# Performance work log

Hardware: AMD Instinct MI355X
Metric: run time of the kernel (lower is better)

Reference implementation:

```python
import jax, jax.numpy as jnp
import numpy as np

KS = 3          # kernel_size
NUM_FA = 16     # number of functional atoms per pixel
TOTAL_BASES = 6 # num_bases * (ks // 2)
BN_EPS = 1e-5


def _conv3x3(x, w, b):
    # NCHW conv, padding=1, stride=1
    y = jax.lax.conv_general_dilated(
        x, w, window_strides=(1, 1), padding=[(1, 1), (1, 1)],
        dimension_numbers=("NCHW", "OIHW", "NCHW"))
    return y + b[None, :, None, None]


def _bn(x, gamma, beta, mean, var):
    scale = gamma / jnp.sqrt(var + BN_EPS)
    return (x - mean[None, :, None, None]) * scale[None, :, None, None] + beta[None, :, None, None]


def setup_inputs() -> dict:
    key = jax.random.key(0)
    ks = jax.random.split(key, 16)
    N, C, H, W = 16, 64, 64, 64
    INTER, BC_DIM, O = 64, TOTAL_BASES * NUM_FA, 128
    f32 = jnp.float32
    return {
        "x": jax.random.normal(ks[0], (N, C, H, W), f32),
        "conv1_w": jax.random.normal(ks[1], (INTER, C, 3, 3), f32) * 0.05,
        "conv1_b": jax.random.normal(ks[2], (INTER,), f32) * 0.05,
        "bn1_gamma": jax.random.uniform(ks[3], (INTER,), f32, 0.5, 1.5),
        "bn1_beta": jax.random.normal(ks[4], (INTER,), f32) * 0.05,
        "bn1_mean": jax.random.normal(ks[5], (INTER,), f32) * 0.05,
        "bn1_var": jax.random.uniform(ks[6], (INTER,), f32, 0.5, 1.5),
        "conv2_w": jax.random.normal(ks[7], (BC_DIM, INTER, 3, 3), f32) * 0.05,
        "conv2_b": jax.random.normal(ks[8], (BC_DIM,), f32) * 0.05,
        "bn2_gamma": jax.random.uniform(ks[9], (BC_DIM,), f32, 0.5, 1.5),
        "bn2_beta": jax.random.normal(ks[10], (BC_DIM,), f32) * 0.05,
        "bn2_mean": jax.random.normal(ks[11], (BC_DIM,), f32) * 0.05,
        "bn2_var": jax.random.uniform(ks[12], (BC_DIM,), f32, 0.5, 1.5),
        "bases": jax.random.normal(ks[13], (TOTAL_BASES, KS * KS), f32),
        "coef": jax.random.normal(ks[14], (O, C * NUM_FA), f32) * 0.02,
    }


def reference(x, conv1_w, conv1_b, bn1_gamma, bn1_beta, bn1_mean, bn1_var,
              conv2_w, conv2_b, bn2_gamma, bn2_beta, bn2_mean, bn2_var,
              bases, coef):
    N, C, H, W = x.shape
    # bases_net: conv3x3 -> BN -> tanh -> conv3x3 -> BN -> tanh
    h = jnp.tanh(_bn(_conv3x3(x, conv1_w, conv1_b), bn1_gamma, bn1_beta, bn1_mean, bn1_var))
    bc = jnp.tanh(_bn(_conv3x3(h, conv2_w, conv2_b), bn2_gamma, bn2_beta, bn2_mean, bn2_var))
    # torch: .transpose(1,-1).view(N,H,W,num_fa,total_bases)  (swaps H/W; H==W)
    bases_coef = jnp.transpose(bc, (0, 3, 2, 1)).reshape(N, H, W, NUM_FA, TOTAL_BASES)
    # atoms: (bases_coef[...,None] * bases).sum(-2).transpose(-1,-2) -> (N,H,W,ks2,num_fa)
    atoms = jnp.einsum("nhwft,tk->nhwkf", bases_coef, bases)
    # unfold(x, ks, padding=1) -> patches (N,H,W,C,ks2), channel-major like torch unfold
    xp = jnp.pad(x, ((0, 0), (0, 0), (1, 1), (1, 1)))
    patches = jnp.stack([xp[:, :, i:i + H, j:j + W] for i in range(KS) for j in range(KS)], axis=2)  # (N,C,9,H,W)
    patches = jnp.transpose(patches, (0, 3, 4, 1, 2))  # (N,H,W,C,9)
    # (x.unsqueeze(-1) * atoms.unsqueeze(-3)).sum(-2) -> (N,H,W,C,num_fa) -> flatten C-major
    bases_out = jnp.einsum("nhwck,nhwkf->nhwcf", patches, atoms).reshape(N, H, W, C * NUM_FA)
    # torch: .transpose(1,-1) -> (N, C*num_fa, W, H), then 1x1 conv with coef
    out = jnp.einsum("nhwd,od->nowh", bases_out, coef)  # (N, O, W, H)
    return out
```

## Files before the change

### kernel.cpp

```cpp
#include <hip/hip_runtime.h>
#include <math.h>
#include <string.h>

#define NBATCH 16

typedef __attribute__((ext_vector_type(8))) short short8;
typedef __attribute__((ext_vector_type(4))) float floatx4;
typedef __fp16 half2v __attribute__((ext_vector_type(2)));
#define MFMA16(a, b, c) __builtin_amdgcn_mfma_f32_16x16x32_bf16(a, b, c, 0, 0, 0)

__device__ __forceinline__ unsigned int cvtpk(float a, float b) {
  unsigned int r;
  asm("v_cvt_pk_bf16_f32 %0, %1, %2" : "=v"(r) : "v"(a), "v"(b));
  return r;
}
__device__ __forceinline__ unsigned short f2bf(float f) {
  return (unsigned short)(cvtpk(f, 0.f) & 0xffffu);
}
__device__ __forceinline__ unsigned int packbf2(float a, float b) {
  return cvtpk(a, b);
}
__device__ __forceinline__ float bflo(unsigned int u) {
  return __uint_as_float(u << 16);
}
__device__ __forceinline__ float bfhi(unsigned int u) {
  return __uint_as_float(u & 0xffff0000u);
}
__device__ __forceinline__ float fast_tanh(float x) {
  float e = __expf(2.f * x);
  return 1.f - 2.f / (e + 1.f);
}

__global__ void prep_weights(const float* __restrict__ w1,
                             const float* __restrict__ w2,
                             const float* __restrict__ coef,
                             unsigned short* __restrict__ w1swz,
                             unsigned short* __restrict__ w2swz,
                             unsigned short* __restrict__ coefswz) {
  int i = blockIdx.x * 256 + threadIdx.x;
  if (i < 131072) {
    int j = i & 7, f = i >> 3;
    int lane = f & 63;
    int u = (f >> 6) & 3;
    int wj = (f >> 8) & 1;
    int kc = (f >> 9) & 1;
    int rd = f >> 10;
    int lm = lane & 15, lq = lane >> 4;
    int oc = wj * 64 + u * 16 + lm;
    int k = rd * 64 + kc * 32 + lq * 8 + j;
    coefswz[i] = f2bf(coef[oc * 1024 + k]);
  }
  if (i < 36864) {
    int j = i & 7, f = i >> 3;
    int lane = f & 63;
    int u = (f >> 6) & 1;
    int wn = (f >> 7) & 1;
    int kc = (f >> 8) & 1;
    int off = f >> 9;
    int lm = lane & 15, lq = lane >> 4;
    int oc = wn * 32 + u * 16 + lm;
    int ic = kc * 32 + lq * 8 + j;
    w1swz[i] = f2bf(w1[(oc * 64 + ic) * 9 + off]);
  }
  if (i < 55296) {
    int j = i & 7, f = i >> 3;
    int lane = f & 63;
    int rem = f >> 6;
    int u = rem % 3;
    int rem2 = rem / 3;
    int wn = rem2 & 1;
    int kc = (rem2 >> 1) & 1;
    int off = rem2 >> 2;
    int lm = lane & 15, lq = lane >> 4;
    int oc = wn * 48 + u * 16 + lm;
    int ic = kc * 32 + lq * 8 + j;
    w2swz[i] = f2bf(w2[(oc * 64 + ic) * 9 + off]);
  }
}

__global__ __launch_bounds__(256) void xb_prep(const float* __restrict__ x,
                                               unsigned short* __restrict__ xb) {
  __shared__ float tile[64][65];
  const int t = threadIdx.x;
  const int y = blockIdx.x, n = blockIdx.y;
  const float* xn = x + (size_t)n * 64 * 4096 + y * 64;
#pragma unroll
  for (int it = 0; it < 16; ++it) {
    int idx = it * 256 + t;
    int c = idx >> 6, xx = idx & 63;
    tile[c][xx] = xn[c * 4096 + xx];
  }
  __syncthreads();
  const int xx = t >> 2, cq = t & 3;
  unsigned short* dst = xb + ((size_t)n * 4096 + y * 64 + xx) * 64;
#pragma unroll
  for (int jj = 0; jj < 2; ++jj) {
    int ch0 = cq * 16 + jj * 8;
    unsigned int p[4];
#pragma unroll
    for (int e = 0; e < 4; ++e)
      p[e] = packbf2(tile[ch0 + e * 2][xx], tile[ch0 + e * 2 + 1][xx]);
    *(uint4*)&dst[ch0] = make_uint4(p[0], p[1], p[2], p[3]);
  }
}

__global__ __launch_bounds__(256) void fused_conv(
    const unsigned short* __restrict__ xb, const unsigned short* __restrict__ w1swz,
    const unsigned short* __restrict__ w2swz, const float* __restrict__ b1,
    const float* __restrict__ g1, const float* __restrict__ be1,
    const float* __restrict__ m1, const float* __restrict__ v1,
    const float* __restrict__ b2, const float* __restrict__ g2,
    const float* __restrict__ be2, const float* __restrict__ m2,
    const float* __restrict__ v2, unsigned short* __restrict__ bcg) {
  __shared__ unsigned short xls[144 * 72];
  __shared__ unsigned short hls[128 * 72];

  const int t = threadIdx.x;
  const int tile = blockIdx.x, n = blockIdx.y;
  const int x0 = (tile & 7) * 8, y0 = (tile >> 3) * 8;

  const unsigned short* xbn = xb + (size_t)n * 4096 * 64;
#pragma unroll
  for (int it = 0; it < 5; ++it) {
    int idx = it * 256 + t;
    if (idx < 1152) {
      int pos = idx >> 3, u4 = idx & 7;
      int xr = pos / 12, xc = pos - xr * 12;
      int gy = y0 - 2 + xr, gx = x0 - 2 + xc;
      uint4 v = {0u, 0u, 0u, 0u};
      if ((unsigned)gy < 64u && (unsigned)gx < 64u)
        v = *(const uint4*)&xbn[((size_t)gy * 64 + gx) * 64 + u4 * 8];
      *(uint4*)&xls[pos * 72 + u4 * 8] = v;
    }
  }
  __syncthreads();

  const int lane = t & 63, w = t >> 6;
  const int wm = w & 1, wn = w >> 1;
  const int lm = lane & 15, lq = lane >> 4;

  int abase[4];
#pragma unroll
  for (int i = 0; i < 4; ++i) {
    int px = (wm + 2 * i) * 16 + lm;
    if (px > 99) px = 99;
    int hr = px / 10, hc = px - hr * 10;
    abase[i] = (hr * 12 + hc) * 72 + lq * 8;
  }
  floatx4 acc[4][2];
#pragma unroll
  for (int i = 0; i < 4; ++i)
#pragma unroll
    for (int u = 0; u < 2; ++u) acc[i][u] = floatx4{0.f, 0.f, 0.f, 0.f};

#pragma unroll
  for (int step = 0; step < 18; ++step) {
    const int off = step >> 1, kc = step & 1;
    const int di = off / 3, dj = off % 3;
    short8 b[2];
#pragma unroll
    for (int u = 0; u < 2; ++u)
      b[u] = *(const short8*)&w1swz[(off * 512 + kc * 256 + wn * 128 + u * 64 +
                                     lane) * 8];
#pragma unroll
    for (int i = 0; i < 4; ++i) {
      short8 a = *(const short8*)&xls[abase[i] + (di * 12 + dj) * 72 + kc * 32];
      acc[i][0] = MFMA16(a, b[0], acc[i][0]);
      acc[i][1] = MFMA16(a, b[1], acc[i][1]);
    }
  }
  {
    float sc[2], sh[2];
#pragma unroll
    for (int u = 0; u < 2; ++u) {
      int oc = wn * 32 + u * 16 + lm;
      sc[u] = g1[oc] * rsqrtf(v1[oc] + 1e-5f);
      sh[u] = (b1[oc] - m1[oc]) * sc[u] + be1[oc];
    }
#pragma unroll
    for (int i = 0; i < 4; ++i) {
      int px0 = (wm + 2 * i) * 16 + lq * 4;
#pragma unroll
      for (int u = 0; u < 2; ++u) {
        int oc = wn * 32 + u * 16 + lm;
#pragma unroll
        for (int r = 0; r < 4; ++r) {
          int px = px0 + r;
          if (px < 100) {
            int hr = px / 10, hc = px - hr * 10;
            int gy = y0 - 1 + hr, gx = x0 - 1 + hc;
            bool valid = ((unsigned)gy < 64u) && ((unsigned)gx < 64u);
            float val = valid ? fast_tanh(acc[i][u][r] * sc[u] + sh[u]) : 0.f;
            hls[px * 72 + oc] = f2bf(val);
          }
        }
      }
    }
  }
  __syncthreads();

  int hbase[2];
#pragma unroll
  for (int s = 0; s < 2; ++s) {
    int opx = (wm + 2 * s) * 16 + lm;
    int yl = opx >> 3, xl = opx & 7;
    hbase[s] = (yl * 10 + xl) * 72 + lq * 8;
  }
  floatx4 acc2[2][3];
#pragma unroll
  for (int s = 0; s < 2; ++s)
#pragma unroll
    for (int u = 0; u < 3; ++u) acc2[s][u] = floatx4{0.f, 0.f, 0.f, 0.f};

#pragma unroll
  for (int step = 0; step < 18; ++step) {
    const int off = step >> 1, kc = step & 1;
    const int di = off / 3, dj = off % 3;
    short8 b[3];
#pragma unroll
    for (int u = 0; u < 3; ++u)
      b[u] = *(const short8*)&w2swz[(off * 768 + kc * 384 + wn * 192 + u * 64 +
                                     lane) * 8];
#pragma unroll
    for (int s = 0; s < 2; ++s) {
      short8 a = *(const short8*)&hls[hbase[s] + (di * 10 + dj) * 72 + kc * 32];
      acc2[s][0] = MFMA16(a, b[0], acc2[s][0]);
      acc2[s][1] = MFMA16(a, b[1], acc2[s][1]);
      acc2[s][2] = MFMA16(a, b[2], acc2[s][2]);
    }
  }
  {
    float sc[3], sh[3];
#pragma unroll
    for (int u = 0; u < 3; ++u) {
      int oc = wn * 48 + u * 16 + lm;
      sc[u] = g2[oc] * rsqrtf(v2[oc] + 1e-5f);
      sh[u] = (b2[oc] - m2[oc]) * sc[u] + be2[oc];
    }
    unsigned short* bcn = bcg + (size_t)n * 4096 * 96;
#pragma unroll
    for (int s = 0; s < 2; ++s) {
      int opx0 = (wm + 2 * s) * 16 + lq * 4;
#pragma unroll
      for (int u = 0; u < 3; ++u) {
        int oc = wn * 48 + u * 16 + lm;
#pragma unroll
        for (int r = 0; r < 4; ++r) {
          int opx = opx0 + r;
          int y = y0 + (opx >> 3), xx = x0 + (opx & 7);
          bcn[((size_t)y * 64 + xx) * 96 + oc] =
              f2bf(fast_tanh(acc2[s][u][r] * sc[u] + sh[u]));
        }
      }
    }
  }
}

__global__ __launch_bounds__(256, 3) void adconv_final(
    const unsigned short* __restrict__ xb, const unsigned short* __restrict__ bc,
    const float* __restrict__ bases, const unsigned short* __restrict__ coefswz,
    float* __restrict__ out) {
  __shared__ unsigned short xs[100 * 72];
  __shared__ unsigned short As[4 * 1024];

  const int t = threadIdx.x;
  const int tile = blockIdx.x, n = blockIdx.y;
  const int q0 = (tile & 7) * 8, p0 = (tile >> 3) * 8;

  float bs[54];
#pragma unroll
  for (int i = 0; i < 54; ++i) bs[i] = bases[i];

  const unsigned short* xbn = xb + (size_t)n * 4096 * 64;
#pragma unroll
  for (int it = 0; it < 4; ++it) {
    int idx = it * 256 + t;
    if (idx < 800) {
      int pos = idx >> 3, u4 = idx & 7;
      int row = pos / 10, col = pos - row * 10;
      int gp = p0 - 1 + row, gq = q0 - 1 + col;
      uint4 v = {0u, 0u, 0u, 0u};
      if ((unsigned)gp < 64u && (unsigned)gq < 64u)
        v = *(const uint4*)&xbn[((size_t)gp * 64 + gq) * 64 + u4 * 8];
      *(uint4*)&xs[pos * 72 + u4 * 8] = v;
    }
  }

  const int lane = t & 63, w = t >> 6;
  const int lm = lane & 15, lq = lane >> 4;

  const int pxl_b = lane >> 2, fh4 = lane & 3;
  const int px_b = w * 16 + pxl_b;
  const int qx_b = px_b >> 3, py_b = px_b & 7;

  half2v atp[9][2];
  {
    const unsigned short* bp =
        bc + ((size_t)n * 4096 + (q0 + qx_b) * 64 + (p0 + py_b)) * 96 + fh4 * 24;
    float bcv[24];
#pragma unroll
    for (int m = 0; m < 3; ++m) {
      uint4 v = *(const uint4*)(bp + m * 8);
      unsigned int uu[4] = {v.x, v.y, v.z, v.w};
#pragma unroll
      for (int e = 0; e < 4; ++e) {
        bcv[m * 8 + e * 2] = bflo(uu[e]);
        bcv[m * 8 + e * 2 + 1] = bfhi(uu[e]);
      }
    }
#pragma unroll
    for (int j2 = 0; j2 < 2; ++j2)
#pragma unroll
      for (int k = 0; k < 9; ++k) {
        float s0 = 0.f, s1 = 0.f;
#pragma unroll
        for (int tt = 0; tt < 6; ++tt) {
          s0 = fmaf(bcv[(2 * j2) * 6 + tt], bs[tt * 9 + k], s0);
          s1 = fmaf(bcv[(2 * j2 + 1) * 6 + tt], bs[tt * 9 + k], s1);
        }
        atp[k][j2] = __builtin_amdgcn_cvt_pkrtz(s0, s1);
      }
  }

  int pa[9];
#pragma unroll
  for (int i = 0; i < 3; ++i)
#pragma unroll
    for (int j = 0; j < 3; ++j)
      pa[i * 3 + j] = ((py_b + i) * 10 + qx_b + j) * 72;

  floatx4 acc[2][4];
#pragma unroll
  for (int wj = 0; wj < 2; ++wj)
#pragma unroll
    for (int u = 0; u < 4; ++u) acc[wj][u] = floatx4{0.f, 0.f, 0.f, 0.f};

  unsigned short* Asw = &As[w * 1024];

  uint2 qv[9];
  auto qload = [&](int rd) {
    const int coff = rd * 4;
#pragma unroll
    for (int p = 0; p < 9; ++p) qv[p] = *(const uint2*)&xs[pa[p] + coff];
  };
  auto build = [&]() {
    float a[4][4];
    {
      float c0 = bflo(qv[0].x), c1 = bfhi(qv[0].x);
      float c2 = bflo(qv[0].y), c3 = bfhi(qv[0].y);
#pragma unroll
      for (int j2 = 0; j2 < 2; ++j2) {
        float a0 = (float)atp[0][j2].x, a1 = (float)atp[0][j2].y;
        a[0][2 * j2] = c0 * a0;
        a[0][2 * j2 + 1] = c0 * a1;
        a[1][2 * j2] = c1 * a0;
        a[1][2 * j2 + 1] = c1 * a1;
        a[2][2 * j2] = c2 * a0;
        a[2][2 * j2 + 1] = c2 * a1;
        a[3][2 * j2] = c3 * a0;
        a[3][2 * j2 + 1] = c3 * a1;
      }
    }
#pragma unroll
    for (int p = 1; p < 9; ++p) {
      float c0 = bflo(qv[p].x), c1 = bfhi(qv[p].x);
      float c2 = bflo(qv[p].y), c3 = bfhi(qv[p].y);
#pragma unroll
      for (int j2 = 0; j2 < 2; ++j2) {
        float a0 = (float)atp[p][j2].x, a1 = (float)atp[p][j2].y;
        a[0][2 * j2] = fmaf(c0, a0, a[0][2 * j2]);
        a[0][2 * j2 + 1] = fmaf(c0, a1, a[0][2 * j2 + 1]);
        a[1][2 * j2] = fmaf(c1, a0, a[1][2 * j2]);
        a[1][2 * j2 + 1] = fmaf(c1, a1, a[1][2 * j2 + 1]);
        a[2][2 * j2] = fmaf(c2, a0, a[2][2 * j2]);
        a[2][2 * j2 + 1] = fmaf(c2, a1, a[2][2 * j2 + 1]);
        a[3][2 * j2] = fmaf(c3, a0, a[3][2 * j2]);
        a[3][2 * j2 + 1] = fmaf(c3, a1, a[3][2 * j2 + 1]);
      }
    }
#pragma unroll
    for (int cc = 0; cc < 4; ++cc) {
      int g = (cc * 4 + fh4) ^ ((pxl_b & 7) << 1);
      uint2 val;
      val.x = cvtpk(a[cc][0], a[cc][1]);
      val.y = cvtpk(a[cc][2], a[cc][3]);
      *(uint2*)&Asw[pxl_b * 64 + g * 4] = val;
    }
  };

  __syncthreads();
  qload(0);
  build();

  for (int rd = 0; rd < 16; ++rd) {
    short8 Af[2];
#pragma unroll
    for (int kc = 0; kc < 2; ++kc) {
      int u16 = (kc * 4 + lq) ^ (lm & 7);
      Af[kc] = *(const short8*)&Asw[lm * 64 + u16 * 8];
    }
    if (rd < 15) {
      qload(rd + 1);
      build();
    }
    {
      short8 Bf[2][4];
#pragma unroll
      for (int wj = 0; wj < 2; ++wj)
#pragma unroll
        for (int u = 0; u < 4; ++u) {
          int frag = ((rd * 2 + 0) * 2 + wj) * 4 + u;
          Bf[wj][u] = *(const short8*)(coefswz + ((size_t)frag * 64 + lane) * 8);
        }
      __builtin_amdgcn_s_setprio(1);
#pragma unroll
      for (int wj = 0; wj < 2; ++wj)
#pragma unroll
        for (int u = 0; u < 4; ++u)
          acc[wj][u] = MFMA16(Af[0], Bf[wj][u], acc[wj][u]);
      __builtin_amdgcn_s_setprio(0);
    }
    {
      short8 Bf[2][4];
#pragma unroll
      for (int wj = 0; wj < 2; ++wj)
#pragma unroll
        for (int u = 0; u < 4; ++u) {
          int frag = ((rd * 2 + 1) * 2 + wj) * 4 + u;
          Bf[wj][u] = *(const short8*)(coefswz + ((size_t)frag * 64 + lane) * 8);
        }
      __builtin_amdgcn_s_setprio(1);
#pragma unroll
      for (int wj = 0; wj < 2; ++wj)
#pragma unroll
        for (int u = 0; u < 4; ++u)
          acc[wj][u] = MFMA16(Af[1], Bf[wj][u], acc[wj][u]);
      __builtin_amdgcn_s_setprio(0);
    }
  }

  float* outn = out + (size_t)n * 128 * 4096;
#pragma unroll
  for (int wj = 0; wj < 2; ++wj)
#pragma unroll
    for (int u = 0; u < 4; ++u) {
      int oc = wj * 64 + u * 16 + lm;
      int gpx = w * 16 + lq * 4;
      int qx = gpx >> 3, py0 = gpx & 7;
      *(float4*)&outn[((size_t)oc * 64 + q0 + qx) * 64 + p0 + py0] =
          make_float4(acc[wj][u][0], acc[wj][u][1], acc[wj][u][2],
                      acc[wj][u][3]);
    }
}

extern "C" void kernel_launch(void* const* d_in, const int* in_sizes, int n_in,
                              void* d_out, int out_size, void* d_ws,
                              size_t ws_size, hipStream_t stream) {
  const float* x = (const float*)d_in[0];
  const float* conv1_w = (const float*)d_in[1];
  const float* conv1_b = (const float*)d_in[2];
  const float* bn1_g = (const float*)d_in[3];
  const float* bn1_b = (const float*)d_in[4];
  const float* bn1_m = (const float*)d_in[5];
  const float* bn1_v = (const float*)d_in[6];
  const float* conv2_w = (const float*)d_in[7];
  const float* conv2_b = (const float*)d_in[8];
  const float* bn2_g = (const float*)d_in[9];
  const float* bn2_b = (const float*)d_in[10];
  const float* bn2_m = (const float*)d_in[11];
  const float* bn2_v = (const float*)d_in[12];
  const float* bases = (const float*)d_in[13];
  const float* coef = (const float*)d_in[14];
  float* out = (float*)d_out;

  char* ws = (char*)d_ws;
  unsigned short* xbuf = (unsigned short*)(ws);
  unsigned short* bcb = (unsigned short*)(ws + 8388608);
  unsigned short* w1swz = (unsigned short*)(ws + 20971520);
  unsigned short* w2swz = (unsigned short*)(ws + 21045248);
  unsigned short* coefswz = (unsigned short*)(ws + 21155840);

  prep_weights<<<512, 256, 0, stream>>>(conv1_w, conv2_w, coef, w1swz, w2swz,
                                        coefswz);
  xb_prep<<<dim3(64, NBATCH), 256, 0, stream>>>(x, xbuf);
  fused_conv<<<dim3(64, NBATCH), 256, 0, stream>>>(
      xbuf, w1swz, w2swz, conv1_b, bn1_g, bn1_b, bn1_m, bn1_v, conv2_b, bn2_g,
      bn2_b, bn2_m, bn2_v, bcb);
  adconv_final<<<dim3(64, NBATCH), 256, 0, stream>>>(xbuf, bcb, bases, coefswz,
                                                     out);
}
```

Before: 169.1 us.

## Keep atoms in fp32 registers and hoist all coef fragment loads per round

In the final adaptive-conv kernel the per-pixel atoms are now stored as 36 fp32 values instead of packed fp16 pairs, which removes per-use fp16-to-fp32 conversions in the patch build. All 16 B-fragment global loads for a round are issued at the top of the loop, before the LDS A reads and the next build, so their latency overlaps the build work. The launch bound is lowered from 3 to 2 blocks per SM to leave room for the extra registers. The trade-off is lower occupancy in exchange for fewer conversions and earlier memory issue.

```diff
diff --git a/kernel.cpp b/kernel.cpp
--- a/kernel.cpp
+++ b/kernel.cpp
@@ -256,7 +256,7 @@
   }
 }
 
-__global__ __launch_bounds__(256, 3) void adconv_final(
+__global__ __launch_bounds__(256, 2) void adconv_final(
     const unsigned short* __restrict__ xb, const unsigned short* __restrict__ bc,
     const float* __restrict__ bases, const unsigned short* __restrict__ coefswz,
     float* __restrict__ out) {
@@ -293,7 +293,7 @@
   const int px_b = w * 16 + pxl_b;
   const int qx_b = px_b >> 3, py_b = px_b & 7;
 
-  half2v atp[9][2];
+  float atf[9][4];
   {
     const unsigned short* bp =
         bc + ((size_t)n * 4096 + (q0 + qx_b) * 64 + (p0 + py_b)) * 96 + fh4 * 24;
@@ -309,16 +309,14 @@
       }
     }
 #pragma unroll
-    for (int j2 = 0; j2 < 2; ++j2)
+    for (int j = 0; j < 4; ++j)
 #pragma unroll
       for (int k = 0; k < 9; ++k) {
-        float s0 = 0.f, s1 = 0.f;
-#pragma unroll
-        for (int tt = 0; tt < 6; ++tt) {
-          s0 = fmaf(bcv[(2 * j2) * 6 + tt], bs[tt * 9 + k], s0);
-          s1 = fmaf(bcv[(2 * j2 + 1) * 6 + tt], bs[tt * 9 + k], s1);
-        }
-        atp[k][j2] = __builtin_amdgcn_cvt_pkrtz(s0, s1);
+        float s0 = 0.f;
+#pragma unroll
+        for (int tt = 0; tt < 6; ++tt)
+          s0 = fmaf(bcv[j * 6 + tt], bs[tt * 9 + k], s0);
+        atf[k][j] = s0;
       }
   }
 
@@ -349,16 +347,12 @@
       float c0 = bflo(qv[0].x), c1 = bfhi(qv[0].x);
       float c2 = bflo(qv[0].y), c3 = bfhi(qv[0].y);
 #pragma unroll
-      for (int j2 = 0; j2 < 2; ++j2) {
-        float a0 = (float)atp[0][j2].x, a1 = (float)atp[0][j2].y;
-        a[0][2 * j2] = c0 * a0;
-        a[0][2 * j2 + 1] = c0 * a1;
-        a[1][2 * j2] = c1 * a0;
-        a[1][2 * j2 + 1] = c1 * a1;
-        a[2][2 * j2] = c2 * a0;
-        a[2][2 * j2 + 1] = c2 * a1;
-        a[3][2 * j2] = c3 * a0;
-        a[3][2 * j2 + 1] = c3 * a1;
+      for (int j = 0; j < 4; ++j) {
+        float av = atf[0][j];
+        a[0][j] = c0 * av;
+        a[1][j] = c1 * av;
+        a[2][j] = c2 * av;
+        a[3][j] = c3 * av;
       }
     }
 #pragma unroll
@@ -366,16 +360,12 @@
       float c0 = bflo(qv[p].x), c1 = bfhi(qv[p].x);
       float c2 = bflo(qv[p].y), c3 = bfhi(qv[p].y);
 #pragma unroll
-      for (int j2 = 0; j2 < 2; ++j2) {
-        float a0 = (float)atp[p][j2].x, a1 = (float)atp[p][j2].y;
-        a[0][2 * j2] = fmaf(c0, a0, a[0][2 * j2]);
-        a[0][2 * j2 + 1] = fmaf(c0, a1, a[0][2 * j2 + 1]);
-        a[1][2 * j2] = fmaf(c1, a0, a[1][2 * j2]);
-        a[1][2 * j2 + 1] = fmaf(c1, a1, a[1][2 * j2 + 1]);
-        a[2][2 * j2] = fmaf(c2, a0, a[2][2 * j2]);
-        a[2][2 * j2 + 1] = fmaf(c2, a1, a[2][2 * j2 + 1]);
-        a[3][2 * j2] = fmaf(c3, a0, a[3][2 * j2]);
-        a[3][2 * j2 + 1] = fmaf(c3, a1, a[3][2 * j2 + 1]);
+      for (int j = 0; j < 4; ++j) {
+        float av = atf[p][j];
+        a[0][j] = fmaf(c0, av, a[0][j]);
+        a[1][j] = fmaf(c1, av, a[1][j]);
+        a[2][j] = fmaf(c2, av, a[2][j]);
+        a[3][j] = fmaf(c3, av, a[3][j]);
       }
     }
 #pragma unroll
@@ -393,6 +383,17 @@
   build();
 
   for (int rd = 0; rd < 16; ++rd) {
+    short8 Bf[2][2][4];
+#pragma unroll
+    for (int kc = 0; kc < 2; ++kc)
+#pragma unroll
+      for (int wj = 0; wj < 2; ++wj)
+#pragma unroll
+        for (int u = 0; u < 4; ++u) {
+          int frag = ((rd * 2 + kc) * 2 + wj) * 4 + u;
+          Bf[kc][wj][u] =
+              *(const short8*)(coefswz + ((size_t)frag * 64 + lane) * 8);
+        }
     short8 Af[2];
 #pragma unroll
     for (int kc = 0; kc < 2; ++kc) {
@@ -403,40 +404,15 @@
       qload(rd + 1);
       build();
     }
-    {
-      short8 Bf[2][4];
+    __builtin_amdgcn_s_setprio(1);
+#pragma unroll
+    for (int kc = 0; kc < 2; ++kc)
 #pragma unroll
       for (int wj = 0; wj < 2; ++wj)
 #pragma unroll
-        for (int u = 0; u < 4; ++u) {
-          int frag = ((rd * 2 + 0) * 2 + wj) * 4 + u;
-          Bf[wj][u] = *(const short8*)(coefswz + ((size_t)frag * 64 + lane) * 8);
-        }
-      __builtin_amdgcn_s_setprio(1);
-#pragma unroll
-      for (int wj = 0; wj < 2; ++wj)
-#pragma unroll
         for (int u = 0; u < 4; ++u)
-          acc[wj][u] = MFMA16(Af[0], Bf[wj][u], acc[wj][u]);
-      __builtin_amdgcn_s_setprio(0);
-    }
-    {
-      short8 Bf[2][4];
-#pragma unroll
-      for (int wj = 0; wj < 2; ++wj)
-#pragma unroll
-        for (int u = 0; u < 4; ++u) {
-          int frag = ((rd * 2 + 1) * 2 + wj) * 4 + u;
-          Bf[wj][u] = *(const short8*)(coefswz + ((size_t)frag * 64 + lane) * 8);
-        }
-      __builtin_amdgcn_s_setprio(1);
-#pragma unroll
-      for (int wj = 0; wj < 2; ++wj)
-#pragma unroll
-        for (int u = 0; u < 4; ++u)
-          acc[wj][u] = MFMA16(Af[1], Bf[wj][u], acc[wj][u]);
-      __builtin_amdgcn_s_setprio(0);
-    }
+          acc[wj][u] = MFMA16(Af[kc], Bf[kc][wj][u], acc[wj][u]);
+    __builtin_amdgcn_s_setprio(0);
   }
 
   float* outn = out + (size_t)n * 128 * 4096;
```

Result: no change. 170.5 us (+0.8%).
